# Performance work log

Hardware: AMD Instinct MI355X
Metric: run time of the kernel (lower is better)

## Reference

```python
import jax, jax.numpy as jnp
import numpy as np

N_NODES = 50000
N_EDGES = 800000
NUM_GRAPHS = 16
NUM_CLASSES = 247


def _glorot(key, shape):
    fan_in = shape[0]
    return jax.random.normal(key, shape, jnp.float32) * (1.0 / np.sqrt(fan_in))


def setup_inputs() -> dict:
    key = jax.random.key(0)
    ks = jax.random.split(key, 8)
    x = jax.random.normal(ks[0], (N_NODES, 3), jnp.float32)
    edge_index = jax.random.randint(ks[1], (2, N_EDGES), 0, N_NODES, dtype=jnp.int64 if jax.config.jax_enable_x64 else jnp.int32)
    batch = jnp.sort(jax.random.randint(ks[2], (N_NODES,), 0, NUM_GRAPHS))
    return {
        "x": x,
        "edge_index": edge_index,
        "batch": batch,
        "W1": _glorot(ks[3], (3, 64)),
        "b1": jnp.zeros((64,), jnp.float32),
        "W2": _glorot(ks[4], (64, 128)),
        "b2": jnp.zeros((128,), jnp.float32),
        "W3": _glorot(ks[5], (128, 256)),
        "b3": jnp.zeros((256,), jnp.float32),
        "Wfc": _glorot(ks[6], (256, NUM_CLASSES)),
        "bfc": jnp.zeros((NUM_CLASSES,), jnp.float32),
    }


def reference(x, edge_index, batch, W1, b1, W2, b2, W3, b3, Wfc, bfc):
    N = x.shape[0]
    # --- GCN symmetric normalization with self-loops (PyG gcn_norm) ---
    loops = jnp.arange(N, dtype=edge_index.dtype)
    ei = jnp.concatenate([edge_index, jnp.stack([loops, loops])], axis=1)
    row, col = ei[0], ei[1]  # src -> dst, aggregate at dst
    deg = jax.ops.segment_sum(jnp.ones(ei.shape[1], x.dtype), col, num_segments=N)
    dinv = jnp.where(deg > 0, jax.lax.rsqrt(deg), 0.0)
    norm = dinv[row] * dinv[col]  # [E+N]

    def gcn(h, W, b):
        h = h @ W                                    # [N, out]
        msg = h[row] * norm[:, None]                 # gather + scale
        agg = jax.ops.segment_sum(msg, col, num_segments=N)  # scatter-add
        return agg + b

    h = jax.nn.relu(gcn(x, W1, b1))
    h = jax.nn.relu(gcn(h, W2, b2))
    h = jax.nn.relu(gcn(h, W3, b3))

    # --- global_mean_pool over batch indices ---
    sums = jax.ops.segment_sum(h, batch, num_segments=NUM_GRAPHS)      # [G, 256]
    cnt = jax.ops.segment_sum(jnp.ones(N, h.dtype), batch, num_segments=NUM_GRAPHS)
    pooled = sums / jnp.maximum(cnt, 1.0)[:, None]

    return pooled @ Wfc + bfc  # [G, num_classes]
```

## Files before the change

kernel.cpp:

```cpp
#include <hip/hip_runtime.h>

#define N_NODES 50000
#define N_EDGES 800000
#define NUM_GRAPHS 16
#define NUM_CLASSES 247
#define SCAN_BLOCKS ((N_NODES + 255) / 256)
#define CSR_CAP (N_EDGES + 7 * N_NODES)

typedef __attribute__((ext_vector_type(8))) short bf16x8;
typedef __attribute__((ext_vector_type(4))) float f32x4;
typedef __attribute__((ext_vector_type(2))) float f32x2;

#if __has_builtin(__builtin_amdgcn_cvt_pk_f32_fp8) && __has_builtin(__builtin_amdgcn_cvt_pk_fp8_f32)
#define HW_FP8 1
#else
#define HW_FP8 0
#endif

static inline int nblk(long n) { return (int)((n + 255) / 256); }

__device__ __forceinline__ float bfl(unsigned short u) {
    return __uint_as_float((unsigned)u << 16);
}
__device__ __forceinline__ unsigned short bf16_rne(float f) {
    unsigned u = __float_as_uint(f);
    u += 0x7FFF + ((u >> 16) & 1);
    return (unsigned short)(u >> 16);
}

__device__ __forceinline__ unsigned q8(float v) {
    if (v < 0.015625f) return 0u;
    unsigned u = __float_as_uint(v) - (120u << 23);
    u += 0x3FFFF + ((u >> 19) & 1);
    unsigned q = u >> 19;
    return q > 255u ? 255u : q;
}
__device__ __forceinline__ float dq8(unsigned x) {
    float f = __uint_as_float((x + 1920u) << 19);
    return x ? f : 0.0f;
}

__device__ __forceinline__ void dq2(unsigned v, float& lo, float& hi) {
#if HW_FP8
    f32x2 t = __builtin_amdgcn_cvt_pk_f32_fp8((int)v, false);
    lo = t[0];
    hi = t[1];
#else
    lo = dq8(v & 0xff);
    hi = dq8(v >> 8);
#endif
}
__device__ __forceinline__ float dq1(unsigned v) {
#if HW_FP8
    f32x2 t = __builtin_amdgcn_cvt_pk_f32_fp8((int)(v & 0xff), false);
    return t[0];
#else
    return dq8(v & 0xff);
#endif
}
__device__ __forceinline__ unsigned enc1(float v) {
#if HW_FP8
    return (unsigned)__builtin_amdgcn_cvt_pk_fp8_f32(v, 0.0f, 0, false) & 0xffu;
#else
    return q8(v);
#endif
}
__device__ __forceinline__ unsigned enc4(float a, float b, float c, float d) {
#if HW_FP8
    int r = __builtin_amdgcn_cvt_pk_fp8_f32(a, b, 0, false);
    r = __builtin_amdgcn_cvt_pk_fp8_f32(c, d, r, true);
    return (unsigned)r;
#else
    return q8(a) | (q8(b) << 8) | (q8(c) << 16) | (q8(d) << 24);
#endif
}

__global__ void k_deg(const int* __restrict__ col, int* __restrict__ degc,
                      int* __restrict__ pos, float* __restrict__ psum,
                      unsigned char* __restrict__ X, unsigned char* __restrict__ Y,
                      int E) {
    if (blockIdx.x == 0) {
        for (int i = threadIdx.x; i < NUM_GRAPHS * 256 + NUM_GRAPHS; i += 256)
            psum[i] = 0.0f;
        if (threadIdx.x < 64) X[(size_t)N_NODES * 64 + threadIdx.x] = 0;
        if (threadIdx.x < 128) Y[(size_t)N_NODES * 128 + threadIdx.x] = 0;
    }
    int e = blockIdx.x * blockDim.x + threadIdx.x;
    if (e >= E) return;
    int c8 = (e >> 8) & 7;
    pos[e] = atomicAdd(&degc[c8 * N_NODES + col[e]], 1);
}

__global__ __launch_bounds__(256) void k_scan1(const int* __restrict__ degc,
                                               int* __restrict__ rowptr,
                                               int* __restrict__ bsum,
                                               const int* __restrict__ batch,
                                               float* __restrict__ pcnt, int N) {
    __shared__ int buf[256];
    __shared__ int hist[NUM_GRAPHS];
    int t = threadIdx.x;
    if (t < NUM_GRAPHS) hist[t] = 0;
    __syncthreads();
    int i = blockIdx.x * 256 + t;
    int v = 0;
    if (i < N) {
        int tot = 0;
#pragma unroll
        for (int c = 0; c < 8; ++c) tot += degc[c * N_NODES + i];
        v = (tot + 7) & ~7;
        atomicAdd(&hist[batch[i]], 1);
    }
    buf[t] = v;
    __syncthreads();
#pragma unroll
    for (int off = 1; off < 256; off <<= 1) {
        int tmp = (t >= off) ? buf[t - off] : 0;
        __syncthreads();
        if (t >= off) buf[t] += tmp;
        __syncthreads();
    }
    if (i < N) rowptr[i] = buf[t] - v;
    if (t == 255) bsum[blockIdx.x] = buf[255];
    if (t < NUM_GRAPHS && hist[t] > 0) atomicAdd(&pcnt[t], (float)hist[t]);
}

__global__ __launch_bounds__(256) void k_scan3(int* __restrict__ rowptr,
                                               const int* __restrict__ bsum,
                                               const int* __restrict__ degc,
                                               int* __restrict__ base,
                                               float* __restrict__ dinv,
                                               const float* __restrict__ x,
                                               float* __restrict__ xs,
                                               int* __restrict__ csr,
                                               const float* __restrict__ W2,
                                               const float* __restrict__ W3,
                                               unsigned short* __restrict__ Wt2,
                                               unsigned short* __restrict__ Wt3,
                                               int N) {
    __shared__ int red[256];
    int t = threadIdx.x;
    int b = blockIdx.x;
    red[t] = (t < b) ? bsum[t] : 0;
    __syncthreads();
#pragma unroll
    for (int off = 128; off > 0; off >>= 1) {
        if (t < off) red[t] += red[t + off];
        __syncthreads();
    }
    int boff = red[0];
    int i = b * 256 + t;
    if (i < N) {
        int rp = rowptr[i] + boff;
        rowptr[i] = rp;
        int run = rp, tot = 0;
#pragma unroll
        for (int c = 0; c < 8; ++c) {
            int d = degc[c * N_NODES + i];
            base[c * N_NODES + i] = run;
            run += d;
            tot += d;
        }
        int pdeg = (tot + 7) & ~7;
        for (int j = rp + tot; j < rp + pdeg; ++j) csr[j] = N_NODES;
        if (i == N - 1) rowptr[N] = rp + pdeg;
        float dv = rsqrtf((float)tot + 1.0f);
        dinv[i] = dv;
        xs[i * 3 + 0] = dv * x[i * 3 + 0];
        xs[i * 3 + 1] = dv * x[i * 3 + 1];
        xs[i * 3 + 2] = dv * x[i * 3 + 2];
    }
    if (i == 0) {
        xs[3 * N_NODES + 0] = 0.0f;
        xs[3 * N_NODES + 1] = 0.0f;
        xs[3 * N_NODES + 2] = 0.0f;
    }
    if (i < 64 * 128) {
        int f = i / 64, k = i % 64;
        Wt2[i] = bf16_rne(W2[k * 128 + f] * 0.015625f);
    } else if (i < 64 * 128 + 128 * 256) {
        int j = i - 64 * 128;
        int f = j / 128, k = j % 128;
        Wt3[j] = bf16_rne(W3[k * 256 + f] * 0.015625f);
    }
}

__global__ void k_fill(const int* __restrict__ row, const int* __restrict__ col,
                       const int* __restrict__ base, const int* __restrict__ pos,
                       int* __restrict__ csr_src, int E) {
    int e = blockIdx.x * blockDim.x + threadIdx.x;
    if (e >= E) return;
    int c8 = (e >> 8) & 7;
    csr_src[base[c8 * N_NODES + col[e]] + pos[e]] = row[e];
}

__global__ void k_layer1(const float* __restrict__ xs, const float* __restrict__ dinv,
                         const int* __restrict__ rowptr, const int* __restrict__ csr_src,
                         const float* __restrict__ W1, const float* __restrict__ b1,
                         unsigned char* __restrict__ out, int N) {
    int v = blockIdx.x * blockDim.x + threadIdx.x;
    if (v >= N) return;
    float a0 = xs[v * 3 + 0];
    float a1 = xs[v * 3 + 1];
    float a2 = xs[v * 3 + 2];
    int j = rowptr[v];
    int j1 = rowptr[v + 1];
    for (; j + 4 <= j1; j += 4) {
        int r0 = csr_src[j + 0], r1 = csr_src[j + 1];
        int r2 = csr_src[j + 2], r3 = csr_src[j + 3];
        float x00 = xs[r0 * 3 + 0], x01 = xs[r0 * 3 + 1], x02 = xs[r0 * 3 + 2];
        float x10 = xs[r1 * 3 + 0], x11 = xs[r1 * 3 + 1], x12 = xs[r1 * 3 + 2];
        float x20 = xs[r2 * 3 + 0], x21 = xs[r2 * 3 + 1], x22 = xs[r2 * 3 + 2];
        float x30 = xs[r3 * 3 + 0], x31 = xs[r3 * 3 + 1], x32 = xs[r3 * 3 + 2];
        a0 += x00; a1 += x01; a2 += x02;
        a0 += x10; a1 += x11; a2 += x12;
        a0 += x20; a1 += x21; a2 += x22;
        a0 += x30; a1 += x31; a2 += x32;
    }
    for (; j < j1; ++j) {
        int r = csr_src[j];
        a0 += xs[r * 3 + 0];
        a1 += xs[r * 3 + 1];
        a2 += xs[r * 3 + 2];
    }
    float dv = dinv[v];
    float p0 = dv * a0, p1 = dv * a1, p2 = dv * a2;
    float dv64 = dv * 64.0f;
    unsigned char* ov = out + (long)v * 64;
#pragma unroll
    for (int f = 0; f < 64; f += 4) {
        float s[4];
#pragma unroll
        for (int t = 0; t < 4; ++t) {
            float sv = fmaf(p0, W1[f + t],
                       fmaf(p1, W1[64 + f + t],
                       fmaf(p2, W1[128 + f + t], b1[f + t])));
            s[t] = fmaxf(sv, 0.0f) * dv64;
        }
        *(unsigned*)(ov + f) = enc4(s[0], s[1], s[2], s[3]);
    }
}

template <int K, int F, bool PRESCALE, bool POOL>
__global__ __launch_bounds__(256, 4) void k_fused(
        const unsigned char* __restrict__ h, const float* __restrict__ dinv,
        const int* __restrict__ rowptr, const int* __restrict__ csr_src,
        const unsigned short* __restrict__ Wt, const float* __restrict__ b,
        unsigned char* __restrict__ out, const int* __restrict__ batch,
        float* __restrict__ psum, int N) {
    constexpr int NF = F / 16;
    constexpr int FPW = NF / 4;
    constexpr int KB = K / 32;
    constexpr int KL = K / 64;
    constexpr int PADK = K + 8;
    __shared__ unsigned short plds[16][PADK];
    int wave = threadIdx.x >> 6;
    int lane = threadIdx.x & 63;
    int m0 = blockIdx.x * 16;

    int vr = m0 + wave * 4;
    float acc[4][KL];
    int j[4], j1[4];
#pragma unroll
    for (int r = 0; r < 4; ++r) {
        const unsigned char* hv = h + (long)(vr + r) * K + lane * KL;
        if (KL == 2) {
            unsigned u = *(const unsigned short*)hv;
            dq2(u, acc[r][0], acc[r][1]);
        } else {
            acc[r][0] = dq1(hv[0]);
        }
        j[r]  = __builtin_amdgcn_readfirstlane(rowptr[vr + r]);
        j1[r] = __builtin_amdgcn_readfirstlane(rowptr[vr + r + 1]);
    }
    while ((j[0] < j1[0]) || (j[1] < j1[1]) || (j[2] < j1[2]) || (j[3] < j1[3])) {
        bool act[4];
        int idx[4][8];
        unsigned tv[4][8];
#pragma unroll
        for (int r = 0; r < 4; ++r) {
            act[r] = j[r] < j1[r];
            if (act[r]) {
#pragma unroll
                for (int u = 0; u < 8; ++u) idx[r][u] = csr_src[j[r] + u];
            }
        }
#pragma unroll
        for (int r = 0; r < 4; ++r) {
            if (act[r]) {
                if (KL == 2) {
#pragma unroll
                    for (int u = 0; u < 8; ++u)
                        tv[r][u] = *(const unsigned short*)(h + (long)idx[r][u] * K + lane * 2);
                } else {
#pragma unroll
                    for (int u = 0; u < 8; ++u)
                        tv[r][u] = h[(long)idx[r][u] * K + lane];
                }
            }
        }
#pragma unroll
        for (int r = 0; r < 4; ++r) {
            if (act[r]) {
                if (KL == 2) {
#pragma unroll
                    for (int u = 0; u < 8; ++u) {
                        float lo, hi;
                        dq2(tv[r][u], lo, hi);
                        acc[r][0] += lo;
                        acc[r][1] += hi;
                    }
                } else {
#pragma unroll
                    for (int u = 0; u < 8; ++u) acc[r][0] += dq1(tv[r][u]);
                }
                j[r] += 8;
            }
        }
    }
#pragma unroll
    for (int r = 0; r < 4; ++r) {
        float dv = dinv[vr + r];
        int rla = wave * 4 + r;
        if (KL == 2) {
            unsigned p = (unsigned)bf16_rne(dv * acc[r][0]) |
                         ((unsigned)bf16_rne(dv * acc[r][1]) << 16);
            *(unsigned*)&plds[rla][lane * 2] = p;
        } else {
            plds[rla][lane] = bf16_rne(dv * acc[r][0]);
        }
    }
    __syncthreads();

    int quad = lane >> 4;
    int l16 = lane & 15;
    bf16x8 afr[KB];
#pragma unroll
    for (int kb = 0; kb < KB; ++kb)
        afr[kb] = *(const bf16x8*)(const void*)&plds[l16][kb * 32 + quad * 8];
#pragma unroll
    for (int fi = 0; fi < FPW; ++fi) {
        int f0 = (wave * FPW + fi) * 16;
        const unsigned short* wrow = Wt + (long)(f0 + l16) * K + quad * 8;
        f32x4 acc4 = {0.f, 0.f, 0.f, 0.f};
#pragma unroll
        for (int kb = 0; kb < KB; ++kb) {
            bf16x8 bb = *(const bf16x8*)(const void*)(wrow + kb * 32);
            acc4 = __builtin_amdgcn_mfma_f32_16x16x32_bf16(afr[kb], bb, acc4, 0, 0, 0);
        }
        float bias = b[f0 + l16];
        if (POOL) {
            int g0 = batch[m0];
            int g15 = batch[m0 + 15];
            if (g0 == g15) {
                float s = fmaxf(acc4[0] + bias, 0.0f);
                s += fmaxf(acc4[1] + bias, 0.0f);
                s += fmaxf(acc4[2] + bias, 0.0f);
                s += fmaxf(acc4[3] + bias, 0.0f);
                s += __shfl_xor(s, 16);
                s += __shfl_xor(s, 32);
                if (quad == 0) atomicAdd(&psum[g0 * 256 + f0 + l16], s);
            } else {
#pragma unroll
                for (int r = 0; r < 4; ++r) {
                    int m = m0 + quad * 4 + r;
                    float val = fmaxf(acc4[r] + bias, 0.0f);
                    atomicAdd(&psum[batch[m] * 256 + f0 + l16], val);
                }
            }
        } else {
#pragma unroll
            for (int r = 0; r < 4; ++r) {
                int m = m0 + quad * 4 + r;
                float val = fmaxf(acc4[r] + bias, 0.0f);
                if (PRESCALE) val *= dinv[m] * 64.0f;
                out[(long)m * F + f0 + l16] = (unsigned char)enc1(val);
            }
        }
    }
}

__global__ void k_fc(const float* __restrict__ psum, const float* __restrict__ pcnt,
                     const float* __restrict__ Wfc, const float* __restrict__ bfc,
                     float* __restrict__ out) {
    int tid = blockIdx.x * blockDim.x + threadIdx.x;
    if (tid >= NUM_GRAPHS * NUM_CLASSES) return;
    int g = tid / NUM_CLASSES;
    int c = tid % NUM_CLASSES;
    float s = 0.0f;
#pragma unroll 8
    for (int k = 0; k < 256; ++k) s = fmaf(psum[g * 256 + k], Wfc[k * NUM_CLASSES + c], s);
    float cnt = pcnt[g];
    cnt = cnt > 1.0f ? cnt : 1.0f;
    out[tid] = s / cnt + bfc[c];
}

extern "C" void kernel_launch(void* const* d_in, const int* in_sizes, int n_in,
                              void* d_out, int out_size, void* d_ws, size_t ws_size,
                              hipStream_t stream) {
    const float* x     = (const float*)d_in[0];
    const int*   ei    = (const int*)d_in[1];
    const int*   batch = (const int*)d_in[2];
    const float* W1    = (const float*)d_in[3];
    const float* b1    = (const float*)d_in[4];
    const float* W2    = (const float*)d_in[5];
    const float* b2    = (const float*)d_in[6];
    const float* W3    = (const float*)d_in[7];
    const float* b3    = (const float*)d_in[8];
    const float* Wfc   = (const float*)d_in[9];
    const float* bfc   = (const float*)d_in[10];
    float* out = (float*)d_out;

    const int* row = ei;
    const int* col = ei + N_EDGES;

    unsigned char* ws = (unsigned char*)d_ws;
    float*  xs   = (float*)ws;
    float*  dinv = (float*)(ws + 600016);
    float*  psum = (float*)(ws + 800016);
    float*  pcnt = (float*)(ws + 816400);
    unsigned char* X = ws + 816512;
    unsigned char* Y = ws + 4016640;
    unsigned short* Wt2 = (unsigned short*)(ws + 10416768);
    unsigned short* Wt3 = (unsigned short*)(ws + 10433152);
    int* degc   = (int*)(ws + 10498688);
    int* base   = (int*)(ws + 12098688);
    int* rowptr = (int*)(ws + 13698688);
    int* csrsrc = (int*)(ws + 13898692);
    int* pos    = (int*)(ws + 18498692);
    int* bsum   = (int*)(ws + 21698692);

    hipMemsetAsync(degc, 0, 8 * N_NODES * sizeof(int), stream);

    k_deg<<<nblk(N_EDGES), 256, 0, stream>>>(col, degc, pos, psum, X, Y, N_EDGES);
    k_scan1<<<SCAN_BLOCKS, 256, 0, stream>>>(degc, rowptr, bsum, batch, pcnt, N_NODES);
    k_scan3<<<SCAN_BLOCKS, 256, 0, stream>>>(rowptr, bsum, degc, base, dinv, x, xs,
                                             csrsrc, W2, W3, Wt2, Wt3, N_NODES);
    k_fill<<<nblk(N_EDGES), 256, 0, stream>>>(row, col, base, pos, csrsrc, N_EDGES);

    k_layer1<<<nblk(N_NODES), 256, 0, stream>>>(xs, dinv, rowptr, csrsrc, W1, b1, X, N_NODES);

    int mtiles = N_NODES / 16;

    k_fused<64, 128, true, false><<<mtiles, 256, 0, stream>>>(
        X, dinv, rowptr, csrsrc, Wt2, b2, Y, batch, psum, N_NODES);

    k_fused<128, 256, false, true><<<mtiles, 256, 0, stream>>>(
        Y, dinv, rowptr, csrsrc, Wt3, b3, (unsigned char*)nullptr, batch, psum, N_NODES);

    k_fc<<<nblk(NUM_GRAPHS * NUM_CLASSES), 256, 0, stream>>>(psum, pcnt, Wfc, bfc, out);
}
```

Measured before the change: 236.3 us.

## Pack CSR indices to 16-bit, pad node features to float4, drop pos array

CSR source indices are stored as unsigned short, since node ids fit under 65536, and read two at a time as 32-bit words. This halves index bandwidth in layer1 and both fused layers. The pos array is removed: k_fill now takes slots with an atomicAdd on the per-chunk base counters, which saves a write and a read of 800k ints. Layer-1 features are padded to 16 bytes so each neighbour gather is one float4 load. The cost is nondeterministic ordering within each CSR segment, and the 16-bit packing relies on N_NODES staying below 65536.

```diff
diff --git a/kernel.cpp b/kernel.cpp
--- a/kernel.cpp
+++ b/kernel.cpp
@@ -76,7 +76,7 @@
 }
 
 __global__ void k_deg(const int* __restrict__ col, int* __restrict__ degc,
-                      int* __restrict__ pos, float* __restrict__ psum,
+                      float* __restrict__ psum,
                       unsigned char* __restrict__ X, unsigned char* __restrict__ Y,
                       int E) {
     if (blockIdx.x == 0) {
@@ -88,7 +88,7 @@
     int e = blockIdx.x * blockDim.x + threadIdx.x;
     if (e >= E) return;
     int c8 = (e >> 8) & 7;
-    pos[e] = atomicAdd(&degc[c8 * N_NODES + col[e]], 1);
+    atomicAdd(&degc[c8 * N_NODES + col[e]], 1);
 }
 
 __global__ __launch_bounds__(256) void k_scan1(const int* __restrict__ degc,
@@ -127,11 +127,11 @@
 __global__ __launch_bounds__(256) void k_scan3(int* __restrict__ rowptr,
                                                const int* __restrict__ bsum,
                                                const int* __restrict__ degc,
-                                               int* __restrict__ base,
+                                               int* __restrict__ basecnt,
                                                float* __restrict__ dinv,
                                                const float* __restrict__ x,
                                                float* __restrict__ xs,
-                                               int* __restrict__ csr,
+                                               unsigned short* __restrict__ csr,
                                                const float* __restrict__ W2,
                                                const float* __restrict__ W3,
                                                unsigned short* __restrict__ Wt2,
@@ -156,23 +156,21 @@
 #pragma unroll
         for (int c = 0; c < 8; ++c) {
             int d = degc[c * N_NODES + i];
-            base[c * N_NODES + i] = run;
+            basecnt[c * N_NODES + i] = run;
             run += d;
             tot += d;
         }
         int pdeg = (tot + 7) & ~7;
-        for (int j = rp + tot; j < rp + pdeg; ++j) csr[j] = N_NODES;
+        for (int j = rp + tot; j < rp + pdeg; ++j) csr[j] = (unsigned short)N_NODES;
         if (i == N - 1) rowptr[N] = rp + pdeg;
         float dv = rsqrtf((float)tot + 1.0f);
         dinv[i] = dv;
-        xs[i * 3 + 0] = dv * x[i * 3 + 0];
-        xs[i * 3 + 1] = dv * x[i * 3 + 1];
-        xs[i * 3 + 2] = dv * x[i * 3 + 2];
+        f32x4 xv = {dv * x[i * 3 + 0], dv * x[i * 3 + 1], dv * x[i * 3 + 2], 0.0f};
+        *(f32x4*)(xs + 4 * i) = xv;
     }
     if (i == 0) {
-        xs[3 * N_NODES + 0] = 0.0f;
-        xs[3 * N_NODES + 1] = 0.0f;
-        xs[3 * N_NODES + 2] = 0.0f;
+        f32x4 z = {0.0f, 0.0f, 0.0f, 0.0f};
+        *(f32x4*)(xs + 4 * N) = z;
     }
     if (i < 64 * 128) {
         int f = i / 64, k = i % 64;
@@ -185,45 +183,47 @@
 }
 
 __global__ void k_fill(const int* __restrict__ row, const int* __restrict__ col,
-                       const int* __restrict__ base, const int* __restrict__ pos,
-                       int* __restrict__ csr_src, int E) {
+                       int* __restrict__ basecnt, unsigned short* __restrict__ csr,
+                       int E) {
     int e = blockIdx.x * blockDim.x + threadIdx.x;
     if (e >= E) return;
     int c8 = (e >> 8) & 7;
-    csr_src[base[c8 * N_NODES + col[e]] + pos[e]] = row[e];
+    int slot = atomicAdd(&basecnt[c8 * N_NODES + col[e]], 1);
+    csr[slot] = (unsigned short)row[e];
 }
 
 __global__ void k_layer1(const float* __restrict__ xs, const float* __restrict__ dinv,
-                         const int* __restrict__ rowptr, const int* __restrict__ csr_src,
+                         const int* __restrict__ rowptr,
+                         const unsigned short* __restrict__ csr_src,
                          const float* __restrict__ W1, const float* __restrict__ b1,
                          unsigned char* __restrict__ out, int N) {
     int v = blockIdx.x * blockDim.x + threadIdx.x;
     if (v >= N) return;
-    float a0 = xs[v * 3 + 0];
-    float a1 = xs[v * 3 + 1];
-    float a2 = xs[v * 3 + 2];
+    const unsigned* csr32 = (const unsigned*)csr_src;
+    f32x4 a = *(const f32x4*)(xs + 4 * v);
     int j = rowptr[v];
     int j1 = rowptr[v + 1];
     for (; j + 4 <= j1; j += 4) {
-        int r0 = csr_src[j + 0], r1 = csr_src[j + 1];
-        int r2 = csr_src[j + 2], r3 = csr_src[j + 3];
-        float x00 = xs[r0 * 3 + 0], x01 = xs[r0 * 3 + 1], x02 = xs[r0 * 3 + 2];
-        float x10 = xs[r1 * 3 + 0], x11 = xs[r1 * 3 + 1], x12 = xs[r1 * 3 + 2];
-        float x20 = xs[r2 * 3 + 0], x21 = xs[r2 * 3 + 1], x22 = xs[r2 * 3 + 2];
-        float x30 = xs[r3 * 3 + 0], x31 = xs[r3 * 3 + 1], x32 = xs[r3 * 3 + 2];
-        a0 += x00; a1 += x01; a2 += x02;
-        a0 += x10; a1 += x11; a2 += x12;
-        a0 += x20; a1 += x21; a2 += x22;
-        a0 += x30; a1 += x31; a2 += x32;
+        unsigned p0 = csr32[(j >> 1) + 0];
+        unsigned p1 = csr32[(j >> 1) + 1];
+        int r0 = p0 & 0xFFFFu, r1 = p0 >> 16;
+        int r2 = p1 & 0xFFFFu, r3 = p1 >> 16;
+        f32x4 x0 = *(const f32x4*)(xs + 4 * r0);
+        f32x4 x1 = *(const f32x4*)(xs + 4 * r1);
+        f32x4 x2 = *(const f32x4*)(xs + 4 * r2);
+        f32x4 x3 = *(const f32x4*)(xs + 4 * r3);
+        a[0] += x0[0]; a[1] += x0[1]; a[2] += x0[2];
+        a[0] += x1[0]; a[1] += x1[1]; a[2] += x1[2];
+        a[0] += x2[0]; a[1] += x2[1]; a[2] += x2[2];
+        a[0] += x3[0]; a[1] += x3[1]; a[2] += x3[2];
     }
     for (; j < j1; ++j) {
         int r = csr_src[j];
-        a0 += xs[r * 3 + 0];
-        a1 += xs[r * 3 + 1];
-        a2 += xs[r * 3 + 2];
+        f32x4 xv = *(const f32x4*)(xs + 4 * r);
+        a[0] += xv[0]; a[1] += xv[1]; a[2] += xv[2];
     }
     float dv = dinv[v];
-    float p0 = dv * a0, p1 = dv * a1, p2 = dv * a2;
+    float p0 = dv * a[0], p1 = dv * a[1], p2 = dv * a[2];
     float dv64 = dv * 64.0f;
     unsigned char* ov = out + (long)v * 64;
 #pragma unroll
@@ -243,7 +243,7 @@
 template <int K, int F, bool PRESCALE, bool POOL>
 __global__ __launch_bounds__(256, 4) void k_fused(
         const unsigned char* __restrict__ h, const float* __restrict__ dinv,
-        const int* __restrict__ rowptr, const int* __restrict__ csr_src,
+        const int* __restrict__ rowptr, const unsigned short* __restrict__ csr_src,
         const unsigned short* __restrict__ Wt, const float* __restrict__ b,
         unsigned char* __restrict__ out, const int* __restrict__ batch,
         float* __restrict__ psum, int N) {
@@ -253,6 +253,7 @@
     constexpr int KL = K / 64;
     constexpr int PADK = K + 8;
     __shared__ unsigned short plds[16][PADK];
+    const unsigned* csr32 = (const unsigned*)csr_src;
     int wave = threadIdx.x >> 6;
     int lane = threadIdx.x & 63;
     int m0 = blockIdx.x * 16;
@@ -281,7 +282,11 @@
             act[r] = j[r] < j1[r];
             if (act[r]) {
 #pragma unroll
-                for (int u = 0; u < 8; ++u) idx[r][u] = csr_src[j[r] + u];
+                for (int u = 0; u < 4; ++u) {
+                    unsigned pk = csr32[(j[r] >> 1) + u];
+                    idx[r][2 * u]     = pk & 0xFFFFu;
+                    idx[r][2 * u + 1] = pk >> 16;
+                }
             }
         }
 #pragma unroll
@@ -415,37 +420,36 @@
 
     unsigned char* ws = (unsigned char*)d_ws;
     float*  xs   = (float*)ws;
-    float*  dinv = (float*)(ws + 600016);
-    float*  psum = (float*)(ws + 800016);
-    float*  pcnt = (float*)(ws + 816400);
-    unsigned char* X = ws + 816512;
-    unsigned char* Y = ws + 4016640;
-    unsigned short* Wt2 = (unsigned short*)(ws + 10416768);
-    unsigned short* Wt3 = (unsigned short*)(ws + 10433152);
-    int* degc   = (int*)(ws + 10498688);
-    int* base   = (int*)(ws + 12098688);
-    int* rowptr = (int*)(ws + 13698688);
-    int* csrsrc = (int*)(ws + 13898692);
-    int* pos    = (int*)(ws + 18498692);
-    int* bsum   = (int*)(ws + 21698692);
+    float*  dinv = (float*)(ws + 800128);
+    float*  psum = (float*)(ws + 1000128);
+    float*  pcnt = (float*)(ws + 1016512);
+    unsigned char* X = ws + 1016576;
+    unsigned char* Y = ws + 4216704;
+    unsigned short* Wt2 = (unsigned short*)(ws + 10616832);
+    unsigned short* Wt3 = (unsigned short*)(ws + 10633216);
+    int* degc    = (int*)(ws + 10698752);
+    int* basecnt = (int*)(ws + 12298752);
+    int* rowptr  = (int*)(ws + 13898752);
+    unsigned short* csr16 = (unsigned short*)(ws + 14098816);
+    int* bsum    = (int*)(ws + 16398816);
 
     hipMemsetAsync(degc, 0, 8 * N_NODES * sizeof(int), stream);
 
-    k_deg<<<nblk(N_EDGES), 256, 0, stream>>>(col, degc, pos, psum, X, Y, N_EDGES);
+    k_deg<<<nblk(N_EDGES), 256, 0, stream>>>(col, degc, psum, X, Y, N_EDGES);
     k_scan1<<<SCAN_BLOCKS, 256, 0, stream>>>(degc, rowptr, bsum, batch, pcnt, N_NODES);
-    k_scan3<<<SCAN_BLOCKS, 256, 0, stream>>>(rowptr, bsum, degc, base, dinv, x, xs,
-                                             csrsrc, W2, W3, Wt2, Wt3, N_NODES);
-    k_fill<<<nblk(N_EDGES), 256, 0, stream>>>(row, col, base, pos, csrsrc, N_EDGES);
-
-    k_layer1<<<nblk(N_NODES), 256, 0, stream>>>(xs, dinv, rowptr, csrsrc, W1, b1, X, N_NODES);
+    k_scan3<<<SCAN_BLOCKS, 256, 0, stream>>>(rowptr, bsum, degc, basecnt, dinv, x, xs,
+                                             csr16, W2, W3, Wt2, Wt3, N_NODES);
+    k_fill<<<nblk(N_EDGES), 256, 0, stream>>>(row, col, basecnt, csr16, N_EDGES);
+
+    k_layer1<<<nblk(N_NODES), 256, 0, stream>>>(xs, dinv, rowptr, csr16, W1, b1, X, N_NODES);
 
     int mtiles = N_NODES / 16;
 
     k_fused<64, 128, true, false><<<mtiles, 256, 0, stream>>>(
-        X, dinv, rowptr, csrsrc, Wt2, b2, Y, batch, psum, N_NODES);
+        X, dinv, rowptr, csr16, Wt2, b2, Y, batch, psum, N_NODES);
 
     k_fused<128, 256, false, true><<<mtiles, 256, 0, stream>>>(
-        Y, dinv, rowptr, csrsrc, Wt3, b3, (unsigned char*)nullptr, batch, psum, N_NODES);
+        Y, dinv, rowptr, csr16, Wt3, b3, (unsigned char*)nullptr, batch, psum, N_NODES);
 
     k_fc<<<nblk(NUM_GRAPHS * NUM_CLASSES), 256, 0, stream>>>(psum, pcnt, Wfc, bfc, out);
 }
```

Result: slower. 258.3 us (+9.3%).
